# Performance work log

Measured on AMD Instinct MI355X. Metric: run time of the kernel, lower is better.

## Reference

```python
import jax, jax.numpy as jnp
import numpy as np

K = 9          # kernel_size (search window)
PAD = 4        # padding = (K-1)//2

def setup_inputs() -> dict:
    key = jax.random.key(0)
    k1, k2 = jax.random.split(key)
    B, C, H, W = 16, 512, 38, 68
    feat1 = jax.random.normal(k1, (B, C, H, W), dtype=jnp.float32)
    feat2 = jax.random.normal(k2, (B, C, H, W), dtype=jnp.float32)
    return {"feat1": feat1, "feat2": feat2}

def reference(feat1, feat2):
    # corr[b,c,k,h,w] = feat1[b,c,h,w] * feat2_pad[b,c,h+dy,w+dx]; output = max over the
    # K*K window offsets k. We compute the max incrementally over the 81 fixed offsets
    # instead of materializing the [B,C,81,H,W] unfold tensor (same math, less memory).
    B, C, H, W = feat1.shape
    f2 = jnp.pad(feat2, ((0, 0), (0, 0), (PAD, PAD), (PAD, PAD)))
    out = None
    for dy in range(K):
        for dx in range(K):
            corr = feat1 * f2[:, :, dy:dy + H, dx:dx + W]  # [B,C,H,W]
            out = corr if out is None else jnp.maximum(out, corr)
    return out
```

## Files before the change

### kernel.cpp

```cpp
#include <hip/hip_runtime.h>


#define HH 38
#define WW 68
#define PLANE (HH * WW)
#define ST 76
#define TPB 384
#define PPB 2
#define NB ((16 * 512) / PPB)

#define BAR() do { asm volatile("s_waitcnt lgkmcnt(0)" ::: "memory"); \
                   __builtin_amdgcn_s_barrier();                      \
                   __builtin_amdgcn_sched_barrier(0); } while (0)

__device__ __forceinline__ float2 f2max(float2 a, float2 b) {
    return make_float2(fmaxf(a.x, b.x), fmaxf(a.y, b.y));
}
__device__ __forceinline__ float2 f2min(float2 a, float2 b) {
    return make_float2(fminf(a.x, b.x), fminf(a.y, b.y));
}

__global__ __launch_bounds__(TPB) void corr_ilp2_kernel(
    const float* __restrict__ f1, const float* __restrict__ f2,
    float* __restrict__ out)
{
    __shared__ float hmx[PPB][HH * ST];
    __shared__ float hmn[PPB][HH * ST];

    const int t = threadIdx.x;
    const int base0 = blockIdx.x * (PPB * PLANE);

    const int hr = t / 9, hs = t % 9;
    const int hc0 = (hs < 8) ? hs * 8 : 60;
    const bool hAct = (t < 342);

    const int vp = t / 170, vj = t % 170;
    const int vcp = vj % 34, vseg = vj / 34;
    const int vc2 = vcp * 2;
    const int vh0 = (vseg < 4) ? vseg * 8 : 30;
    const bool vAct = (t < 340);

    float2 v[16];
    if (vAct) {
        const float* fp = f2 + base0 + vp * PLANE;
        #pragma unroll
        for (int i = 0; i < 16; ++i) {
            int row = vh0 - 4 + i;
            v[i] = (row >= 0 && row < HH)
                 ? *reinterpret_cast<const float2*>(fp + row * WW + vc2)
                 : make_float2(0.0f, 0.0f);
        }
    }

    float4 fa0, fb0;
    if (hAct) {
        fa0 = *reinterpret_cast<const float4*>(f1 + base0 + hr * WW + hc0);
        fb0 = *reinterpret_cast<const float4*>(f1 + base0 + hr * WW + hc0 + 4);
    }

    if (t < 304) {
        int row = t >> 3, q = t & 7;
        int side = q & 1, quant = (q >> 1) & 1, pl = q >> 2;
        float* b = quant ? hmn[pl] : hmx[pl];
        *reinterpret_cast<float4*>(b + row * ST + (side ? 72 : 0)) =
            make_float4(0, 0, 0, 0);
    }

    if (vAct) {
        float* bx = hmx[vp];
        float* bn = hmn[vp];
        float2 S[9], P;
        S[8] = v[8];
        #pragma unroll
        for (int i = 7; i >= 0; --i) S[i] = f2max(v[i], S[i + 1]);
        *reinterpret_cast<float2*>(bx + vh0 * ST + 4 + vc2) = S[0];
        P = v[9];
        #pragma unroll
        for (int k = 1; k < 8; ++k) {
            *reinterpret_cast<float2*>(bx + (vh0 + k) * ST + 4 + vc2) = f2max(S[k], P);
            if (k < 7) P = f2max(P, v[9 + k]);
        }
        S[8] = v[8];
        #pragma unroll
        for (int i = 7; i >= 0; --i) S[i] = f2min(v[i], S[i + 1]);
        *reinterpret_cast<float2*>(bn + vh0 * ST + 4 + vc2) = S[0];
        P = v[9];
        #pragma unroll
        for (int k = 1; k < 8; ++k) {
            *reinterpret_cast<float2*>(bn + (vh0 + k) * ST + 4 + vc2) = f2min(S[k], P);
            if (k < 7) P = f2min(P, v[9 + k]);
        }
    }

    BAR();

    float4 fa1, fb1;
    if (hAct) {
        fa1 = *reinterpret_cast<const float4*>(f1 + base0 + PLANE + hr * WW + hc0);
        fb1 = *reinterpret_cast<const float4*>(f1 + base0 + PLANE + hr * WW + hc0 + 4);
    }

    #pragma unroll
    for (int p = 0; p < PPB; ++p) {
        if (hAct) {
            float u[16], S[9], wx[8], wn[8], P;
            #pragma unroll
            for (int q = 0; q < 4; ++q)
                *reinterpret_cast<float4*>(&u[q * 4]) =
                    *reinterpret_cast<const float4*>(&hmx[p][hr * ST + hc0 + q * 4]);
            S[8] = u[8];
            #pragma unroll
            for (int i = 7; i >= 0; --i) S[i] = fmaxf(u[i], S[i + 1]);
            wx[0] = S[0];
            P = u[9];
            #pragma unroll
            for (int k = 1; k < 8; ++k) {
                wx[k] = fmaxf(S[k], P);
                if (k < 7) P = fmaxf(P, u[9 + k]);
            }
            #pragma unroll
            for (int q = 0; q < 4; ++q)
                *reinterpret_cast<float4*>(&u[q * 4]) =
                    *reinterpret_cast<const float4*>(&hmn[p][hr * ST + hc0 + q * 4]);
            S[8] = u[8];
            #pragma unroll
            for (int i = 7; i >= 0; --i) S[i] = fminf(u[i], S[i + 1]);
            wn[0] = S[0];
            P = u[9];
            #pragma unroll
            for (int k = 1; k < 8; ++k) {
                wn[k] = fminf(S[k], P);
                if (k < 7) P = fminf(P, u[9 + k]);
            }
            float4 A = (p == 0) ? fa0 : fa1;
            float4 B = (p == 0) ? fb0 : fb1;
            float4 ra, rb;
            ra.x = A.x * (A.x >= 0.0f ? wx[0] : wn[0]);
            ra.y = A.y * (A.y >= 0.0f ? wx[1] : wn[1]);
            ra.z = A.z * (A.z >= 0.0f ? wx[2] : wn[2]);
            ra.w = A.w * (A.w >= 0.0f ? wx[3] : wn[3]);
            rb.x = B.x * (B.x >= 0.0f ? wx[4] : wn[4]);
            rb.y = B.y * (B.y >= 0.0f ? wx[5] : wn[5]);
            rb.z = B.z * (B.z >= 0.0f ? wx[6] : wn[6]);
            rb.w = B.w * (B.w >= 0.0f ? wx[7] : wn[7]);
            *reinterpret_cast<float4*>(out + base0 + p * PLANE + hr * WW + hc0)     = ra;
            *reinterpret_cast<float4*>(out + base0 + p * PLANE + hr * WW + hc0 + 4) = rb;
        }
    }
}

extern "C" void kernel_launch(void* const* d_in, const int* in_sizes, int n_in,
                              void* d_out, int out_size, void* d_ws, size_t ws_size,
                              hipStream_t stream) {
    const float* f1 = (const float*)d_in[0];
    const float* f2 = (const float*)d_in[1];
    float* out = (float*)d_out;
    corr_ilp2_kernel<<<dim3(NB), dim3(TPB), 0, stream>>>(f1, f2, out);
}
```

Measured before the change: 45.10 us.

## Assign one wavefront per plane with banded LDS processing and no block barriers

Restructures the kernel so each 64-lane wavefront owns a whole channel plane and processes it in four row bands, using a small per-wave LDS buffer. Block-level s_barrier synchronisation is replaced by wave-local lgkmcnt fences, and LDS use drops sharply, which raises possible occupancy. In exchange, the four bands run serially within a wave, so there is less memory-level parallelism per wave and f1 loads are issued later, next to their use.

```diff
diff --git a/kernel.cpp b/kernel.cpp
--- a/kernel.cpp
+++ b/kernel.cpp
@@ -4,14 +4,13 @@
 #define HH 38
 #define WW 68
 #define PLANE (HH * WW)
-#define ST 76
-#define TPB 384
-#define PPB 2
-#define NB ((16 * 512) / PPB)
+#define ST 84
+#define NR 10
+#define TPB 256
+#define NB 2048
 
-#define BAR() do { asm volatile("s_waitcnt lgkmcnt(0)" ::: "memory"); \
-                   __builtin_amdgcn_s_barrier();                      \
-                   __builtin_amdgcn_sched_barrier(0); } while (0)
+#define FENCE() do { asm volatile("s_waitcnt lgkmcnt(0)" ::: "memory"); \
+                     __builtin_amdgcn_sched_barrier(0); } while (0)
 
 __device__ __forceinline__ float2 f2max(float2 a, float2 b) {
     return make_float2(fmaxf(a.x, b.x), fmaxf(a.y, b.y));
@@ -20,120 +19,87 @@
     return make_float2(fminf(a.x, b.x), fminf(a.y, b.y));
 }
 
-__global__ __launch_bounds__(TPB) void corr_ilp2_kernel(
-    const float* __restrict__ f1, const float* __restrict__ f2,
-    float* __restrict__ out)
+template <int H0, int NRr, int ILO, int IHI>
+__device__ __forceinline__ void do_band(
+    const int l, const int base,
+    const float* __restrict__ f1, const float* __restrict__ fp,
+    float* __restrict__ out,
+    float (*__restrict__ bx)[ST], float (*__restrict__ bn)[ST])
 {
-    __shared__ float hmx[PPB][HH * ST];
-    __shared__ float hmn[PPB][HH * ST];
-
-    const int t = threadIdx.x;
-    const int base0 = blockIdx.x * (PPB * PLANE);
-
-    const int hr = t / 9, hs = t % 9;
-    const int hc0 = (hs < 8) ? hs * 8 : 60;
-    const bool hAct = (t < 342);
-
-    const int vp = t / 170, vj = t % 170;
-    const int vcp = vj % 34, vseg = vj / 34;
-    const int vc2 = vcp * 2;
-    const int vh0 = (vseg < 4) ? vseg * 8 : 30;
-    const bool vAct = (t < 340);
-
-    float2 v[16];
-    if (vAct) {
-        const float* fp = f2 + base0 + vp * PLANE;
+    if (l < 34) {
+        const int c2 = 2 * l;
+        float2 v[NRr + 8];
         #pragma unroll
-        for (int i = 0; i < 16; ++i) {
-            int row = vh0 - 4 + i;
-            v[i] = (row >= 0 && row < HH)
-                 ? *reinterpret_cast<const float2*>(fp + row * WW + vc2)
+        for (int i = 0; i < NRr + 8; ++i) {
+            v[i] = (i >= ILO && i <= IHI)
+                 ? *reinterpret_cast<const float2*>(fp + (H0 - 4 + i) * WW + c2)
                  : make_float2(0.0f, 0.0f);
         }
-    }
-
-    float4 fa0, fb0;
-    if (hAct) {
-        fa0 = *reinterpret_cast<const float4*>(f1 + base0 + hr * WW + hc0);
-        fb0 = *reinterpret_cast<const float4*>(f1 + base0 + hr * WW + hc0 + 4);
-    }
-
-    if (t < 304) {
-        int row = t >> 3, q = t & 7;
-        int side = q & 1, quant = (q >> 1) & 1, pl = q >> 2;
-        float* b = quant ? hmn[pl] : hmx[pl];
-        *reinterpret_cast<float4*>(b + row * ST + (side ? 72 : 0)) =
-            make_float4(0, 0, 0, 0);
-    }
-
-    if (vAct) {
-        float* bx = hmx[vp];
-        float* bn = hmn[vp];
         float2 S[9], P;
         S[8] = v[8];
         #pragma unroll
         for (int i = 7; i >= 0; --i) S[i] = f2max(v[i], S[i + 1]);
-        *reinterpret_cast<float2*>(bx + vh0 * ST + 4 + vc2) = S[0];
+        *reinterpret_cast<float2*>(&bx[0][4 + c2]) = S[0];
         P = v[9];
         #pragma unroll
-        for (int k = 1; k < 8; ++k) {
-            *reinterpret_cast<float2*>(bx + (vh0 + k) * ST + 4 + vc2) = f2max(S[k], P);
-            if (k < 7) P = f2max(P, v[9 + k]);
+        for (int k = 1; k < NRr; ++k) {
+            float2 o = (k <= 8) ? f2max(S[k], P) : P;
+            *reinterpret_cast<float2*>(&bx[k][4 + c2]) = o;
+            if (9 + k < NRr + 8) P = f2max(P, v[9 + k]);
         }
         S[8] = v[8];
         #pragma unroll
         for (int i = 7; i >= 0; --i) S[i] = f2min(v[i], S[i + 1]);
-        *reinterpret_cast<float2*>(bn + vh0 * ST + 4 + vc2) = S[0];
+        *reinterpret_cast<float2*>(&bn[0][4 + c2]) = S[0];
         P = v[9];
         #pragma unroll
-        for (int k = 1; k < 8; ++k) {
-            *reinterpret_cast<float2*>(bn + (vh0 + k) * ST + 4 + vc2) = f2min(S[k], P);
-            if (k < 7) P = f2min(P, v[9 + k]);
+        for (int k = 1; k < NRr; ++k) {
+            float2 o = (k <= 8) ? f2min(S[k], P) : P;
+            *reinterpret_cast<float2*>(&bn[k][4 + c2]) = o;
+            if (9 + k < NRr + 8) P = f2min(P, v[9 + k]);
         }
     }
 
-    BAR();
-
-    float4 fa1, fb1;
-    if (hAct) {
-        fa1 = *reinterpret_cast<const float4*>(f1 + base0 + PLANE + hr * WW + hc0);
-        fb1 = *reinterpret_cast<const float4*>(f1 + base0 + PLANE + hr * WW + hc0 + 4);
-    }
+    FENCE();
 
     #pragma unroll
-    for (int p = 0; p < PPB; ++p) {
-        if (hAct) {
-            float u[16], S[9], wx[8], wn[8], P;
+    for (int it = 0; it < 2; ++it) {
+        const int ji = l + it * 64;
+        if (ji < NRr * 9) {
+            const int row = ji / 9, seg = ji % 9;
+            const int hc0 = (seg < 8) ? seg * 8 : 60;
+            float u[16], S[9], wx[8], wn[8], Pp;
             #pragma unroll
             for (int q = 0; q < 4; ++q)
                 *reinterpret_cast<float4*>(&u[q * 4]) =
-                    *reinterpret_cast<const float4*>(&hmx[p][hr * ST + hc0 + q * 4]);
+                    *reinterpret_cast<const float4*>(&bx[row][hc0 + q * 4]);
             S[8] = u[8];
             #pragma unroll
             for (int i = 7; i >= 0; --i) S[i] = fmaxf(u[i], S[i + 1]);
             wx[0] = S[0];
-            P = u[9];
+            Pp = u[9];
             #pragma unroll
             for (int k = 1; k < 8; ++k) {
-                wx[k] = fmaxf(S[k], P);
-                if (k < 7) P = fmaxf(P, u[9 + k]);
+                wx[k] = fmaxf(S[k], Pp);
+                if (k < 7) Pp = fmaxf(Pp, u[9 + k]);
             }
             #pragma unroll
             for (int q = 0; q < 4; ++q)
                 *reinterpret_cast<float4*>(&u[q * 4]) =
-                    *reinterpret_cast<const float4*>(&hmn[p][hr * ST + hc0 + q * 4]);
+                    *reinterpret_cast<const float4*>(&bn[row][hc0 + q * 4]);
             S[8] = u[8];
             #pragma unroll
             for (int i = 7; i >= 0; --i) S[i] = fminf(u[i], S[i + 1]);
             wn[0] = S[0];
-            P = u[9];
+            Pp = u[9];
             #pragma unroll
             for (int k = 1; k < 8; ++k) {
-                wn[k] = fminf(S[k], P);
-                if (k < 7) P = fminf(P, u[9 + k]);
+                wn[k] = fminf(S[k], Pp);
+                if (k < 7) Pp = fminf(Pp, u[9 + k]);
             }
-            float4 A = (p == 0) ? fa0 : fa1;
-            float4 B = (p == 0) ? fb0 : fb1;
+            const float* f1r = f1 + base + (H0 + row) * WW + hc0;
+            float4 A = *reinterpret_cast<const float4*>(f1r);
+            float4 B = *reinterpret_cast<const float4*>(f1r + 4);
             float4 ra, rb;
             ra.x = A.x * (A.x >= 0.0f ? wx[0] : wn[0]);
             ra.y = A.y * (A.y >= 0.0f ? wx[1] : wn[1]);
@@ -143,10 +109,40 @@
             rb.y = B.y * (B.y >= 0.0f ? wx[5] : wn[5]);
             rb.z = B.z * (B.z >= 0.0f ? wx[6] : wn[6]);
             rb.w = B.w * (B.w >= 0.0f ? wx[7] : wn[7]);
-            *reinterpret_cast<float4*>(out + base0 + p * PLANE + hr * WW + hc0)     = ra;
-            *reinterpret_cast<float4*>(out + base0 + p * PLANE + hr * WW + hc0 + 4) = rb;
+            float* outp = out + base + (H0 + row) * WW + hc0;
+            *reinterpret_cast<float4*>(outp)     = ra;
+            *reinterpret_cast<float4*>(outp + 4) = rb;
         }
     }
+
+    FENCE();
+}
+
+__global__ __launch_bounds__(TPB) void corr_wave_kernel(
+    const float* __restrict__ f1, const float* __restrict__ f2,
+    float* __restrict__ out)
+{
+    __shared__ float lds[TPB / 64][2][NR][ST];
+
+    const int t = threadIdx.x;
+    const int w = t >> 6, l = t & 63;
+    float (*bx)[ST] = lds[w][0];
+    float (*bn)[ST] = lds[w][1];
+
+    const int plane = blockIdx.x * (TPB / 64) + w;
+    const int base  = plane * PLANE;
+    const float* fp = f2 + base;
+
+    if (l < 40) {
+        int q = l & 1, side = (l >> 1) & 1, r = l >> 2;
+        *reinterpret_cast<float4*>(&lds[w][q][r][side ? 72 : 0]) =
+            make_float4(0, 0, 0, 0);
+    }
+
+    do_band< 0, 10, 4, 17>(l, base, f1, fp, out, bx, bn);
+    do_band<10, 10, 0, 17>(l, base, f1, fp, out, bx, bn);
+    do_band<20, 10, 0, 17>(l, base, f1, fp, out, bx, bn);
+    do_band<30,  8, 0, 11>(l, base, f1, fp, out, bx, bn);
 }
 
 extern "C" void kernel_launch(void* const* d_in, const int* in_sizes, int n_in,
@@ -155,5 +151,5 @@
     const float* f1 = (const float*)d_in[0];
     const float* f2 = (const float*)d_in[1];
     float* out = (float*)d_out;
-    corr_ilp2_kernel<<<dim3(NB), dim3(TPB), 0, stream>>>(f1, f2, out);
+    corr_wave_kernel<<<dim3(NB), dim3(TPB), 0, stream>>>(f1, f2, out);
 }
```

New measurement: 49.64 us. 1.1x slower.
